# Kernel tuning notes

Hardware: AMD Instinct MI355X
Metric: run time of the kernel (lower is better)

The kernel has to match this reference:

```python
import jax, jax.numpy as jnp
import numpy as np

FP8_MAX = 448.0  # max finite value of float8_e4m3fn


def _fp8_quant(v, scale):
    # emulate saturating scaled cast to float8_e4m3fn, then dequant-free fp8 storage (upcast to f32 for the gemm)
    q = jnp.clip(v / scale, -FP8_MAX, FP8_MAX)
    return q.astype(jnp.float8_e4m3fn).astype(jnp.float32)


def setup_inputs() -> dict:
    key = jax.random.key(0)
    k0, k1, k2, k3 = jax.random.split(key, 4)
    T, H, I, E = 1024, 1024, 2816, 8
    x = jax.random.normal(k0, (T, H), jnp.float32)
    router_logits = jax.random.normal(k1, (T, E), jnp.float32)
    w13_weight = jax.random.normal(k2, (E, 2 * I, H), jnp.float32) * 0.02
    w2_weight = jax.random.normal(k3, (E, H, I), jnp.float32) * 0.02
    return {
        "x": x,
        "router_logits": router_logits,
        "w13_weight": w13_weight,
        "w2_weight": w2_weight,
        "w13_input_scale": jnp.ones((E,), jnp.float32),
        "w2_input_scale": jnp.ones((E,), jnp.float32),
        "top_k": 2,
    }


def reference(x, router_logits, w13_weight, w2_weight, w13_input_scale, w2_input_scale, top_k):
    T, H = x.shape
    E, two_I, _ = w13_weight.shape
    I = two_I // 2

    # --- routing: softmax -> top_k -> renormalize (select_experts) ---
    probs = jax.nn.softmax(router_logits, axis=-1)
    topk_w, topk_ids = jax.lax.top_k(probs, top_k)            # [T,K]
    topk_w = topk_w / jnp.sum(topk_w, axis=-1, keepdims=True)
    # dense combine matrix [T,E]: sparsity of the grouped gemm dispatch
    combine = jnp.zeros((T, E), x.dtype).at[jnp.arange(T)[:, None], topk_ids].add(topk_w)

    # --- per-expert fp8 weight quantization (ops.scaled_fp8_quant per expert) ---
    w13_scale = jnp.max(jnp.abs(w13_weight), axis=(1, 2)) / FP8_MAX  # [E]
    w2_scale = jnp.max(jnp.abs(w2_weight), axis=(1, 2)) / FP8_MAX
    w13_q = _fp8_quant(w13_weight, w13_scale[:, None, None])         # [E,2I,H]
    w2_q = _fp8_quant(w2_weight, w2_scale[:, None, None])            # [E,H,I]

    # --- grouped gemm 1: per-expert activation quant + fp8 gemm + dequant scale ---
    x_q = _fp8_quant(x[None], w13_input_scale[:, None, None])        # [E,T,H]
    h = jnp.einsum('eth,eih->eti', x_q, w13_q) * (w13_input_scale * w13_scale)[:, None, None]

    # --- silu_and_mul: gate = first intermediate_size rows, up = second ---
    act = jax.nn.silu(h[..., :I]) * h[..., I:]                       # [E,T,I]

    # --- grouped gemm 2 ---
    act_q = _fp8_quant(act, w2_input_scale[:, None, None])
    o = jnp.einsum('eti,ehi->eth', act_q, w2_q) * (w2_input_scale * w2_scale)[:, None, None]

    # --- post_reorder: weighted combine of selected experts ---
    return jnp.einsum('te,eth->th', combine, o)                      # [T,H]
```

## Files before the change

### kernel.cpp

```cpp
#include <hip/hip_runtime.h>
#include <cstdint>
#include <cstddef>

#define T_TOK 1024
#define H_DIM 1024
#define I_DIM 2816
#define E_NUM 8
#define PAIRS 2048
#define KSPLIT 4

typedef __attribute__((ext_vector_type(4))) float f32x4;
typedef __attribute__((ext_vector_type(4))) unsigned int u32x4;
typedef long i64;

__device__ __forceinline__ unsigned char fp8e4m3_sw(float v) {
  v = fminf(448.f, fmaxf(-448.f, v));
  unsigned b = __float_as_uint(v);
  unsigned s = (b >> 24) & 0x80u;
  float a = fabsf(v);
  if (a < 0.015625f) {
    int m = (int)rintf(a * 512.f);
    return (unsigned char)(s | (unsigned)m);
  }
  unsigned ab = b & 0x7fffffffu;
  unsigned rnd = 0x7FFFFu + ((ab >> 20) & 1u);
  ab += rnd;
  int e = (int)(ab >> 23) - 127;
  unsigned m = (ab >> 20) & 7u;
  if (e > 8 || (e == 8 && m > 6)) { e = 8; m = 6; }
  return (unsigned char)(s | (unsigned)((e + 7) << 3) | m);
}

__device__ __forceinline__ unsigned q4(float a, float b, float c, float d) {
#if __has_builtin(__builtin_amdgcn_cvt_pk_fp8_f32)
  unsigned w = (unsigned)__builtin_amdgcn_cvt_pk_fp8_f32(a, b, 0, false);
  return (unsigned)__builtin_amdgcn_cvt_pk_fp8_f32(c, d, (int)w, true);
#else
  return (unsigned)fp8e4m3_sw(a) | ((unsigned)fp8e4m3_sw(b) << 8) |
         ((unsigned)fp8e4m3_sw(c) << 16) | ((unsigned)fp8e4m3_sw(d) << 24);
#endif
}

__device__ __forceinline__ unsigned char q1(float a) {
#if __has_builtin(__builtin_amdgcn_cvt_pk_fp8_f32)
  return (unsigned char)((unsigned)__builtin_amdgcn_cvt_pk_fp8_f32(a, a, 0, false) & 0xFFu);
#else
  return fp8e4m3_sw(a);
#endif
}

__device__ __forceinline__ unsigned q4v(float4 f, float inv) {
  return q4(f.x * inv, f.y * inv, f.z * inv, f.w * inv);
}

__global__ __launch_bounds__(1024) void route_k(const float* __restrict__ logits,
                                                unsigned* __restrict__ amax13,
                                                unsigned* __restrict__ amax2,
                                                int* __restrict__ cnt_g,
                                                int* __restrict__ offs_g,
                                                int* __restrict__ pair_tok,
                                                float* __restrict__ pair_w,
                                                int* __restrict__ pairidx) {
  __shared__ int cnt_s[E_NUM], pos_s[E_NUM];
  const int tid = threadIdx.x;
  if (tid < E_NUM) { cnt_s[tid] = 0; amax13[tid] = 0; amax2[tid] = 0; }
  __syncthreads();

  float l[E_NUM];
#pragma unroll
  for (int j = 0; j < E_NUM; j++) l[j] = logits[tid * E_NUM + j];
  int i0 = 0; float b0 = l[0];
#pragma unroll
  for (int j = 1; j < E_NUM; j++) { if (l[j] > b0) { b0 = l[j]; i0 = j; } }
  int i1 = -1; float b1 = -3.4e38f;
#pragma unroll
  for (int j = 0; j < E_NUM; j++) { if (j != i0 && l[j] > b1) { b1 = l[j]; i1 = j; } }
  float e1 = expf(b1 - b0);
  float d = 1.f + e1;
  float w0 = 1.f / d, w1 = e1 / d;

  atomicAdd(&cnt_s[i0], 1);
  atomicAdd(&cnt_s[i1], 1);
  __syncthreads();
  if (tid == 0) {
    int s = 0;
#pragma unroll
    for (int e = 0; e < E_NUM; e++) {
      cnt_g[e] = cnt_s[e];
      offs_g[e] = s;
      pos_s[e] = s;
      s += cnt_s[e];
    }
    offs_g[E_NUM] = s;
  }
  __syncthreads();
  int s0 = atomicAdd(&pos_s[i0], 1);
  pair_tok[s0] = tid; pair_w[s0] = w0; pairidx[2 * tid] = s0;
  int s1 = atomicAdd(&pos_s[i1], 1);
  pair_tok[s1] = tid; pair_w[s1] = w1; pairidx[2 * tid + 1] = s1;
}

__global__ __launch_bounds__(256) void amax_k(const float* __restrict__ w13,
                                              const float* __restrict__ w2,
                                              unsigned* __restrict__ amax13,
                                              unsigned* __restrict__ amax2) {
  const int e = blockIdx.y;
  const float4* src;
  unsigned* dst;
  int bx = blockIdx.x, nb;
  if (bx < 128) { src = (const float4*)w13 + (size_t)e * (2 * I_DIM * H_DIM / 4); dst = &amax13[e]; nb = 128; }
  else          { src = (const float4*)w2  + (size_t)e * (H_DIM * I_DIM / 4);     dst = &amax2[e];  bx -= 128; nb = 64; }
  int idx = bx * 256 + threadIdx.x;
  int stride = nb * 256;
  float m = 0.f;
#pragma unroll
  for (int j = 0; j < 44; j += 4) {
    float4 v0 = src[idx + (size_t)(j + 0) * stride];
    float4 v1 = src[idx + (size_t)(j + 1) * stride];
    float4 v2 = src[idx + (size_t)(j + 2) * stride];
    float4 v3 = src[idx + (size_t)(j + 3) * stride];
    m = fmaxf(m, fmaxf(fmaxf(fabsf(v0.x), fabsf(v0.y)), fmaxf(fabsf(v0.z), fabsf(v0.w))));
    m = fmaxf(m, fmaxf(fmaxf(fabsf(v1.x), fabsf(v1.y)), fmaxf(fabsf(v1.z), fabsf(v1.w))));
    m = fmaxf(m, fmaxf(fmaxf(fabsf(v2.x), fabsf(v2.y)), fmaxf(fabsf(v2.z), fabsf(v2.w))));
    m = fmaxf(m, fmaxf(fmaxf(fabsf(v3.x), fabsf(v3.y)), fmaxf(fabsf(v3.z), fabsf(v3.w))));
  }
#pragma unroll
  for (int off = 32; off > 0; off >>= 1) m = fmaxf(m, __shfl_xor(m, off));
  __shared__ float wmax[4];
  int lane = threadIdx.x & 63, wid = threadIdx.x >> 6;
  if (lane == 0) wmax[wid] = m;
  __syncthreads();
  if (threadIdx.x == 0) {
    float mm = fmaxf(fmaxf(wmax[0], wmax[1]), fmaxf(wmax[2], wmax[3]));
    atomicMax(dst, __float_as_uint(mm));
  }
}

__global__ __launch_bounds__(256) void quantx_k(const float* __restrict__ x,
                                                const int* __restrict__ pair_tok,
                                                const int* __restrict__ offs,
                                                const float* __restrict__ s13,
                                                unsigned char* __restrict__ Xq) {
  int p = blockIdx.x;
  int t = pair_tok[p];
  int e = 0;
#pragma unroll
  for (int j = 1; j < E_NUM; j++) { if (p >= offs[j]) e = j; }
  float inv = 1.f / s13[e];
  float4 v = ((const float4*)(x + (size_t)t * H_DIM))[threadIdx.x];
  float a = fminf(448.f, fmaxf(-448.f, v.x * inv));
  float b = fminf(448.f, fmaxf(-448.f, v.y * inv));
  float c = fminf(448.f, fmaxf(-448.f, v.z * inv));
  float dd = fminf(448.f, fmaxf(-448.f, v.w * inv));
  ((unsigned*)(Xq + (size_t)p * H_DIM))[threadIdx.x] = q4(a, b, c, dd);
}

__global__ __launch_bounds__(512) void gemm1_k(const float* __restrict__ w13,
                                               const unsigned char* __restrict__ Xq,
                                               unsigned char* __restrict__ H1,
                                               const int* __restrict__ cnt,
                                               const int* __restrict__ offs,
                                               const unsigned* __restrict__ amax13,
                                               const float* __restrict__ s13,
                                               const float* __restrict__ s2in) {
  const int e = blockIdx.z;
  const int count = cnt[e];
  const int m0 = blockIdx.y * 256;
  if (m0 >= count) return;
  const int nt = blockIdx.x;
  const int base = offs[e];

  const float amax = __uint_as_float(amax13[e]);
  const float inv_w = 448.f / amax;
  const float gs = s13[e] * (amax / 448.f);
  const float inv_a2 = 1.f / s2in[e];

  __shared__ __align__(16) unsigned char As[256][80];
  __shared__ __align__(16) unsigned char Bs[64][80];

  const int tid = threadIdx.x, lane = tid & 63, wq = tid >> 6;
  const int fr = lane & 15, ks = lane >> 4;

  f32x4 accg[2][2], accu[2][2];
#pragma unroll
  for (int i = 0; i < 2; i++)
#pragma unroll
    for (int j = 0; j < 2; j++) { accg[i][j] = (f32x4)0.f; accu[i][j] = (f32x4)0.f; }

  const int ar0 = tid >> 2, ar1 = (tid + 512) >> 2, aseg = tid & 3;
  int pr0 = base + m0 + ar0; if (pr0 > PAIRS - 1) pr0 = PAIRS - 1;
  int pr1 = base + m0 + ar1; if (pr1 > PAIRS - 1) pr1 = PAIRS - 1;
  const unsigned char* a_src0 = Xq + (size_t)pr0 * H_DIM + aseg * 16;
  const unsigned char* a_src1 = Xq + (size_t)pr1 * H_DIM + aseg * 16;

  const int brow = tid >> 3, bseg = tid & 7;
  const size_t brg = (size_t)nt * 32 + (brow & 31) + (size_t)(brow >> 5) * I_DIM;
  const float* b_src = w13 + ((size_t)e * 2 * I_DIM + brg) * H_DIM + bseg * 8;

  u32x4 ra0 = *(const u32x4*)a_src0;
  u32x4 ra1 = *(const u32x4*)a_src1;
  float4 fb0 = ((const float4*)b_src)[0], fb1 = ((const float4*)b_src)[1];
  unsigned qb0 = q4v(fb0, inv_w), qb1 = q4v(fb1, inv_w);

  for (int t = 0; t < H_DIM / 64; ++t) {
    __syncthreads();
    *(u32x4*)&As[ar0][aseg * 16] = ra0;
    *(u32x4*)&As[ar1][aseg * 16] = ra1;
    ((unsigned*)&Bs[brow][bseg * 8])[0] = qb0;
    ((unsigned*)&Bs[brow][bseg * 8])[1] = qb1;
    __syncthreads();
    if (t + 1 < H_DIM / 64) {
      int k0 = (t + 1) * 64;
      ra0 = *(const u32x4*)(a_src0 + k0);
      ra1 = *(const u32x4*)(a_src1 + k0);
      fb0 = ((const float4*)(b_src + k0))[0];
      fb1 = ((const float4*)(b_src + k0))[1];
    }
#pragma unroll
    for (int kk = 0; kk < 2; kk++) {
      i64 a0 = *(const i64*)&As[wq * 32 + fr][kk * 32 + ks * 8];
      i64 a1 = *(const i64*)&As[wq * 32 + 16 + fr][kk * 32 + ks * 8];
#pragma unroll
      for (int ni = 0; ni < 2; ni++) {
        i64 bg = *(const i64*)&Bs[ni * 16 + fr][kk * 32 + ks * 8];
        i64 bu = *(const i64*)&Bs[32 + ni * 16 + fr][kk * 32 + ks * 8];
        accg[0][ni] = __builtin_amdgcn_mfma_f32_16x16x32_fp8_fp8(a0, bg, accg[0][ni], 0, 0, 0);
        accg[1][ni] = __builtin_amdgcn_mfma_f32_16x16x32_fp8_fp8(a1, bg, accg[1][ni], 0, 0, 0);
        accu[0][ni] = __builtin_amdgcn_mfma_f32_16x16x32_fp8_fp8(a0, bu, accu[0][ni], 0, 0, 0);
        accu[1][ni] = __builtin_amdgcn_mfma_f32_16x16x32_fp8_fp8(a1, bu, accu[1][ni], 0, 0, 0);
      }
    }
    qb0 = q4v(fb0, inv_w);
    qb1 = q4v(fb1, inv_w);
  }

  const int rg = lane >> 4;
#pragma unroll
  for (int mi = 0; mi < 2; mi++) {
#pragma unroll
    for (int rr = 0; rr < 4; rr++) {
      int lrow = wq * 32 + mi * 16 + rg * 4 + rr;
      if (m0 + lrow < count) {
        size_t p = (size_t)(base + m0 + lrow);
#pragma unroll
        for (int ni = 0; ni < 2; ni++) {
          int col = nt * 32 + ni * 16 + fr;
          float g = accg[mi][ni][rr] * gs;
          float u = accu[mi][ni][rr] * gs;
          float act = g / (1.f + expf(-g)) * u * inv_a2;
          act = fminf(448.f, fmaxf(-448.f, act));
          H1[p * I_DIM + col] = q1(act);
        }
      }
    }
  }
}

__global__ __launch_bounds__(512) void gemm2_k(const float* __restrict__ w2,
                                               const unsigned char* __restrict__ H1,
                                               float* __restrict__ Op,
                                               const int* __restrict__ cnt,
                                               const int* __restrict__ offs,
                                               const unsigned* __restrict__ amax2,
                                               const float* __restrict__ s2in,
                                               const float* __restrict__ pair_w) {
  const int e = blockIdx.z;
  const int count = cnt[e];
  const int m0 = blockIdx.y * 128;
  if (m0 >= count) return;
  const int nt = blockIdx.x & 15;
  const int ksp = blockIdx.x >> 4;
  const int n0 = nt * 64;
  const int base = offs[e];

  const float amax = __uint_as_float(amax2[e]);
  const float inv_w = 448.f / amax;
  const float s2 = s2in[e] * (amax / 448.f);

  __shared__ __align__(16) unsigned char As[128][80];
  __shared__ __align__(16) unsigned char Bs[64][80];

  const int tid = threadIdx.x, lane = tid & 63, wq = tid >> 6;
  const int fr = lane & 15, ks = lane >> 4;

  f32x4 acc[4];
#pragma unroll
  for (int i = 0; i < 4; i++) acc[i] = (f32x4)0.f;

  const int arow = tid >> 2, aseg = tid & 3;
  int pr = base + m0 + arow; if (pr > PAIRS - 1) pr = PAIRS - 1;
  const unsigned char* a_src = H1 + (size_t)pr * I_DIM + aseg * 16;

  const int brow = tid >> 3, bseg = tid & 7;
  const float* b_src = w2 + ((size_t)e * H_DIM + n0 + brow) * I_DIM + bseg * 8;

  const int KITER = (I_DIM / 64) / KSPLIT;
  const int kbase = ksp * KITER * 64;

  u32x4 ra = *(const u32x4*)(a_src + kbase);
  float4 fb0 = ((const float4*)(b_src + kbase))[0];
  float4 fb1 = ((const float4*)(b_src + kbase))[1];
  unsigned qb0 = q4v(fb0, inv_w), qb1 = q4v(fb1, inv_w);

  for (int t = 0; t < KITER; ++t) {
    __syncthreads();
    *(u32x4*)&As[arow][aseg * 16] = ra;
    ((unsigned*)&Bs[brow][bseg * 8])[0] = qb0;
    ((unsigned*)&Bs[brow][bseg * 8])[1] = qb1;
    __syncthreads();
    if (t + 1 < KITER) {
      int k0 = kbase + (t + 1) * 64;
      ra = *(const u32x4*)(a_src + k0);
      fb0 = ((const float4*)(b_src + k0))[0];
      fb1 = ((const float4*)(b_src + k0))[1];
    }
#pragma unroll
    for (int kk = 0; kk < 2; kk++) {
      i64 a0 = *(const i64*)&As[wq * 16 + fr][kk * 32 + ks * 8];
#pragma unroll
      for (int ni = 0; ni < 4; ni++) {
        i64 b = *(const i64*)&Bs[ni * 16 + fr][kk * 32 + ks * 8];
        acc[ni] = __builtin_amdgcn_mfma_f32_16x16x32_fp8_fp8(a0, b, acc[ni], 0, 0, 0);
      }
    }
    qb0 = q4v(fb0, inv_w);
    qb1 = q4v(fb1, inv_w);
  }

  const int rg = lane >> 4;
#pragma unroll
  for (int rr = 0; rr < 4; rr++) {
    int lrow = wq * 16 + rg * 4 + rr;
    if (m0 + lrow < count) {
      size_t p = (size_t)(base + m0 + lrow);
      float pw = pair_w[p];
#pragma unroll
      for (int ni = 0; ni < 4; ni++) {
        int col = n0 + ni * 16 + fr;
        Op[((size_t)ksp * PAIRS + p) * H_DIM + col] = acc[ni][rr] * s2 * pw;
      }
    }
  }
}

__global__ __launch_bounds__(256) void combine_k(const float* __restrict__ Op,
                                                 const int* __restrict__ pairidx,
                                                 float* __restrict__ out) {
  int t = blockIdx.x;
  int p0 = pairidx[2 * t], p1 = pairidx[2 * t + 1];
  f32x4 acc = (f32x4)0.f;
#pragma unroll
  for (int s = 0; s < KSPLIT; s++) {
    f32x4 a = ((const f32x4*)(Op + ((size_t)s * PAIRS + p0) * H_DIM))[threadIdx.x];
    f32x4 b = ((const f32x4*)(Op + ((size_t)s * PAIRS + p1) * H_DIM))[threadIdx.x];
    acc += a + b;
  }
  ((f32x4*)(out + (size_t)t * H_DIM))[threadIdx.x] = acc;
}

extern "C" void kernel_launch(void* const* d_in, const int* in_sizes, int n_in,
                              void* d_out, int out_size, void* d_ws, size_t ws_size,
                              hipStream_t stream) {
  (void)in_sizes; (void)n_in; (void)out_size; (void)ws_size;
  const float* x      = (const float*)d_in[0];
  const float* logits = (const float*)d_in[1];
  const float* w13    = (const float*)d_in[2];
  const float* w2     = (const float*)d_in[3];
  const float* s13    = (const float*)d_in[4];
  const float* s2in   = (const float*)d_in[5];
  float* out = (float*)d_out;

  char* ws = (char*)d_ws;
  unsigned* amax13 = (unsigned*)(ws + 0);
  unsigned* amax2  = (unsigned*)(ws + 64);
  int* cnt     = (int*)(ws + 128);
  int* offs    = (int*)(ws + 192);
  int* pair_tok = (int*)(ws + 17408);
  float* pair_w = (float*)(ws + 25600);
  int* pairidx  = (int*)(ws + 33792);
  unsigned char* Xq = (unsigned char*)(ws + (size_t)(1 << 20));
  unsigned char* H1 = (unsigned char*)(ws + (size_t)4 * (1 << 20));
  float* Op         = (float*)(ws + (size_t)10 * (1 << 20));

  route_k<<<1, 1024, 0, stream>>>(logits, amax13, amax2, cnt, offs,
                                  pair_tok, pair_w, pairidx);

  amax_k<<<dim3(192, E_NUM), 256, 0, stream>>>(w13, w2, amax13, amax2);

  quantx_k<<<PAIRS, 256, 0, stream>>>(x, pair_tok, offs, s13, Xq);

  gemm1_k<<<dim3(I_DIM / 32, 4, E_NUM), 512, 0, stream>>>(
      w13, Xq, H1, cnt, offs, amax13, s13, s2in);

  gemm2_k<<<dim3(16 * KSPLIT, 8, E_NUM), 512, 0, stream>>>(
      w2, H1, Op, cnt, offs, amax2, s2in, pair_w);

  combine_k<<<T_TOK, 256, 0, stream>>>(Op, pairidx, out);
}
```

Measured before the change: 171.7 us.

## Move w2 amax reduction into gemm1 launch as extra blocks

The w2 absolute-max reduction is split out of the standalone amax kernel and run as extra blocks appended to the gemm1 grid. The w2 weight scan can then overlap with the gemm1 work instead of running before it. The w13 amax kernel keeps its own launch. In exchange, gemm1 gets a larger grid with many idle blocks (blockIdx.y != 0 returns), and the amax blocks compete with gemm1 for memory bandwidth.

```diff
diff --git a/kernel.cpp b/kernel.cpp
--- a/kernel.cpp
+++ b/kernel.cpp
@@ -8,6 +8,8 @@
 #define E_NUM 8
 #define PAIRS 2048
 #define KSPLIT 4
+#define NT1 (I_DIM / 32)
+#define AMX2_BLKS 128
 
 typedef __attribute__((ext_vector_type(4))) float f32x4;
 typedef __attribute__((ext_vector_type(4))) unsigned int u32x4;
@@ -100,18 +102,12 @@
   pair_tok[s1] = tid; pair_w[s1] = w1; pairidx[2 * tid + 1] = s1;
 }
 
-__global__ __launch_bounds__(256) void amax_k(const float* __restrict__ w13,
-                                              const float* __restrict__ w2,
-                                              unsigned* __restrict__ amax13,
-                                              unsigned* __restrict__ amax2) {
+__global__ __launch_bounds__(256) void amax13_k(const float* __restrict__ w13,
+                                                unsigned* __restrict__ amax13) {
   const int e = blockIdx.y;
-  const float4* src;
-  unsigned* dst;
-  int bx = blockIdx.x, nb;
-  if (bx < 128) { src = (const float4*)w13 + (size_t)e * (2 * I_DIM * H_DIM / 4); dst = &amax13[e]; nb = 128; }
-  else          { src = (const float4*)w2  + (size_t)e * (H_DIM * I_DIM / 4);     dst = &amax2[e];  bx -= 128; nb = 64; }
-  int idx = bx * 256 + threadIdx.x;
-  int stride = nb * 256;
+  const float4* src = (const float4*)w13 + (size_t)e * (2 * I_DIM * H_DIM / 4);
+  int idx = blockIdx.x * 256 + threadIdx.x;
+  int stride = gridDim.x * 256;
   float m = 0.f;
 #pragma unroll
   for (int j = 0; j < 44; j += 4) {
@@ -132,7 +128,7 @@
   __syncthreads();
   if (threadIdx.x == 0) {
     float mm = fmaxf(fmaxf(wmax[0], wmax[1]), fmaxf(wmax[2], wmax[3]));
-    atomicMax(dst, __float_as_uint(mm));
+    atomicMax(&amax13[e], __float_as_uint(mm));
   }
 }
 
@@ -156,14 +152,44 @@
 }
 
 __global__ __launch_bounds__(512) void gemm1_k(const float* __restrict__ w13,
+                                               const float* __restrict__ w2,
                                                const unsigned char* __restrict__ Xq,
                                                unsigned char* __restrict__ H1,
                                                const int* __restrict__ cnt,
                                                const int* __restrict__ offs,
                                                const unsigned* __restrict__ amax13,
+                                               unsigned* __restrict__ amax2,
                                                const float* __restrict__ s13,
                                                const float* __restrict__ s2in) {
   const int e = blockIdx.z;
+
+  if (blockIdx.x >= NT1) {
+    if (blockIdx.y != 0) return;
+    const int bx = blockIdx.x - NT1;
+    const float4* src = (const float4*)w2 + (size_t)e * (H_DIM * I_DIM / 4);
+    int idx = bx * 512 + threadIdx.x;
+    int stride = AMX2_BLKS * 512;
+    float m = 0.f;
+#pragma unroll
+    for (int j = 0; j < 11; j++) {
+      float4 v = src[idx + (size_t)j * stride];
+      m = fmaxf(m, fmaxf(fmaxf(fabsf(v.x), fabsf(v.y)), fmaxf(fabsf(v.z), fabsf(v.w))));
+    }
+#pragma unroll
+    for (int off = 32; off > 0; off >>= 1) m = fmaxf(m, __shfl_xor(m, off));
+    __shared__ float wmax2[8];
+    int lane = threadIdx.x & 63, wid = threadIdx.x >> 6;
+    if (lane == 0) wmax2[wid] = m;
+    __syncthreads();
+    if (threadIdx.x == 0) {
+      float mm = wmax2[0];
+#pragma unroll
+      for (int j = 1; j < 8; j++) mm = fmaxf(mm, wmax2[j]);
+      atomicMax(&amax2[e], __float_as_uint(mm));
+    }
+    return;
+  }
+
   const int count = cnt[e];
   const int m0 = blockIdx.y * 256;
   if (m0 >= count) return;
@@ -385,12 +411,12 @@
   route_k<<<1, 1024, 0, stream>>>(logits, amax13, amax2, cnt, offs,
                                   pair_tok, pair_w, pairidx);
 
-  amax_k<<<dim3(192, E_NUM), 256, 0, stream>>>(w13, w2, amax13, amax2);
+  amax13_k<<<dim3(128, E_NUM), 256, 0, stream>>>(w13, amax13);
 
   quantx_k<<<PAIRS, 256, 0, stream>>>(x, pair_tok, offs, s13, Xq);
 
-  gemm1_k<<<dim3(I_DIM / 32, 4, E_NUM), 512, 0, stream>>>(
-      w13, Xq, H1, cnt, offs, amax13, s13, s2in);
+  gemm1_k<<<dim3(NT1 + AMX2_BLKS, 4, E_NUM), 512, 0, stream>>>(
+      w13, w2, Xq, H1, cnt, offs, amax13, amax2, s13, s2in);
 
   gemm2_k<<<dim3(16 * KSPLIT, 8, E_NUM), 512, 0, stream>>>(
       w2, H1, Op, cnt, offs, amax2, s2in, pair_w);
```

Measured after the change: 165.4 us. 3.7% less time.
